# Kernel tuning notes

Hardware: AMD Instinct MI355X
Metric: run time of the kernel (lower is better)

## Reference

```python
import jax, jax.numpy as jnp
import numpy as np

N = 50000          # number of graph nodes
R = 4              # number of relation types (rt_num)
E = 800000         # edges per relation (avg degree 16)
D_IN = 128
D_OUT = 64
EPS = 1e-12        # torch F.normalize eps


def setup_inputs() -> dict:
    key = jax.random.key(0)
    k1, k2, k3, k4, k5 = jax.random.split(key, 5)
    x = jax.random.normal(k1, (N, D_IN), dtype=jnp.float32)
    W = jax.random.normal(k2, (R, D_IN, D_OUT), dtype=jnp.float32)
    b = jnp.zeros((R, D_OUT), dtype=jnp.float32)
    adj_vals = jax.random.uniform(k3, (R, E), dtype=jnp.float32)
    adj_rows = jax.random.randint(k4, (R, E), 0, N, dtype=jnp.int32)
    adj_cols = jax.random.randint(k5, (R, E), 0, N, dtype=jnp.int32)
    return {"x": x, "W": W, "b": b, "adj_vals": adj_vals,
            "adj_rows": adj_rows, "adj_cols": adj_cols, "dropout": 0}


def reference(x, W, b, adj_vals, adj_rows, adj_cols, dropout):
    # dropout == 0 -> F.dropout is the identity; reference is deterministic.
    # Per-relation dense projection: xw[r] = x @ W[r]   -> [R, N, D_OUT]
    xw = jnp.einsum('nd,rdo->rno', x, W)

    def per_relation(xw_r, rows_r, cols_r, vals_r, b_r):
        # sparse adjacency SpMM: out[i] = sum_e vals[e] * xw[cols[e]] for rows[e]==i
        msg = xw_r[cols_r] * vals_r[:, None]                  # [E, D_OUT] gather
        agg = jax.ops.segment_sum(msg, rows_r, num_segments=N)  # [N, D_OUT] scatter-add
        return jax.nn.relu(agg + b_r)                          # bias + act

    outs = jax.vmap(per_relation)(xw, adj_rows, adj_cols, adj_vals, b)  # [R, N, D_OUT]
    total = jnp.sum(outs, axis=0)                               # cross-relation sum
    # L2 normalize over feature dim (torch F.normalize, dim=1)
    norm = jnp.maximum(jnp.linalg.norm(total, axis=1, keepdims=True), EPS)
    return total / norm
```

## Files before the change

### kernel.cpp

```cpp
#include <hip/hip_runtime.h>
#include <hip/hip_bf16.h>
#include <stdint.h>

#define NN 50000
#define DI 128
#define DO 64
#define NE 800000
#define NR 4
#define NB 782
#define NBUCK (NR*NB)
#define PCHUNK 7168
#define PWG ((NE + PCHUNK - 1) / PCHUNK)
#define RSCAP 4096
#define CONVB 1024
#define GEMMB ((NN + 127) / 128)

typedef short short8 __attribute__((ext_vector_type(8)));
typedef float f32x4  __attribute__((ext_vector_type(4)));
union FragU { uint4 u; short8 s; };

__device__ __forceinline__ uint32_t bfb(float f)
{
    __hip_bfloat16 h = __float2bfloat16(f);
    return (uint32_t)*reinterpret_cast<unsigned short*>(&h);
}

template<int N, int PER, int BLK>
__device__ inline void block_exscan(int* a)
{
    __shared__ int wsum[BLK / 64];
    int tid = threadIdx.x;
    int base = tid * PER;
    int v[PER]; int s = 0;
    #pragma unroll
    for (int j = 0; j < PER; ++j) {
        int idx = base + j;
        int x = (idx < N) ? a[idx] : 0;
        v[j] = s; s += x;
    }
    int lane = tid & 63, wv = tid >> 6;
    int inc = s;
    #pragma unroll
    for (int off = 1; off < 64; off <<= 1) {
        int u = __shfl_up(inc, off);
        if (lane >= off) inc += u;
    }
    if (lane == 63) wsum[wv] = inc;
    __syncthreads();
    int woff = 0;
    for (int w = 0; w < wv; ++w) woff += wsum[w];
    int tb = woff + inc - s;
    #pragma unroll
    for (int j = 0; j < PER; ++j) {
        int idx = base + j;
        if (idx < N) a[idx] = tb + v[j];
    }
}

__global__ __launch_bounds__(256) void prep_kernel(
    const float* __restrict__ x, const float* __restrict__ W,
    const int* __restrict__ rows,
    uint2* __restrict__ xb, uint16_t* __restrict__ wt,
    int* __restrict__ gtot)
{
    __shared__ int h[NB];
    int bid = blockIdx.x, tid = threadIdx.x;

    if (bid < CONVB) {
        const int total = NN * DI / 4;
        const float4* x4 = (const float4*)x;
        for (int i = bid * 256 + tid; i < total; i += CONVB * 256) {
            float4 v = x4[i];
            uint2 o;
            o.x = bfb(v.x) | (bfb(v.y) << 16);
            o.y = bfb(v.z) | (bfb(v.w) << 16);
            xb[i] = o;
        }
    } else if (bid < CONVB + 128) {
        int i = (bid - CONVB) * 256 + tid;
        int r = i >> 13;
        int k = (i >> 6) & 127;
        int n = i & 63;
        wt[((size_t)(r * DO + n) << 7) + k] = (uint16_t)bfb(W[i]);
    } else {
        int bb = bid - (CONVB + 128);
        int r = bb >> 5, sub = bb & 31;
        for (int i = tid; i < NB; i += 256) h[i] = 0;
        __syncthreads();
        const int4* rr4 = (const int4*)(rows + (size_t)r * NE);
        for (int k = sub * 256 + tid; k < NE / 4; k += 32 * 256) {
            int4 v = rr4[k];
            atomicAdd(&h[v.x >> 6], 1);
            atomicAdd(&h[v.y >> 6], 1);
            atomicAdd(&h[v.z >> 6], 1);
            atomicAdd(&h[v.w >> 6], 1);
        }
        __syncthreads();
        int* gt = gtot + r * NB;
        for (int i = tid; i < NB; i += 256)
            if (h[i]) atomicAdd(&gt[i], h[i]);
    }
}

__global__ __launch_bounds__(512) void gemm_bases_kernel(
    const uint4* __restrict__ xb4, const uint4* __restrict__ wt4,
    uint16_t* __restrict__ xwb,
    const int* __restrict__ gtot, int* __restrict__ gstart,
    int* __restrict__ gcur)
{
    __shared__ __align__(16) uint16_t tile[128 * 64];
    __shared__ int a[NBUCK + 1];
    int tid = threadIdx.x;

    if (blockIdx.x == GEMMB) {
        for (int i = tid; i < NBUCK + 1; i += 512)
            a[i] = (i < NBUCK) ? gtot[i] : 0;
        __syncthreads();
        block_exscan<NBUCK + 1, 7, 512>(a);
        __syncthreads();
        for (int i = tid; i < NBUCK + 1; i += 512) {
            gstart[i] = a[i];
            if (i < NBUCK) gcur[i] = a[i];
        }
        return;
    }

    int wv = __builtin_amdgcn_readfirstlane(tid >> 6);
    int lane = tid & 63;
    int n0 = blockIdx.x * 128 + wv * 16;
    int m16 = lane & 15, g = lane >> 4;
    bool act = (n0 < NN);

    FragU af[4];
    if (act) {
        #pragma unroll
        for (int ks = 0; ks < 4; ++ks)
            af[ks].u = xb4[(size_t)(n0 + m16) * 16 + ks * 4 + g];
    }

    int rows = NN - blockIdx.x * 128; if (rows > 128) rows = 128;

    for (int r = 0; r < NR; ++r) {
        if (act) {
            #pragma unroll
            for (int ct = 0; ct < 4; ++ct) {
                f32x4 acc = {0.f, 0.f, 0.f, 0.f};
                #pragma unroll
                for (int ks = 0; ks < 4; ++ks) {
                    FragU b;
                    b.u = wt4[(size_t)((r * DO + ct * 16 + m16) * 16) + ks * 4 + g];
                    acc = __builtin_amdgcn_mfma_f32_16x16x32_bf16(
                        af[ks].s, b.s, acc, 0, 0, 0);
                }
                #pragma unroll
                for (int j = 0; j < 4; ++j)
                    tile[(wv * 16 + g * 4 + j) * 64 + ct * 16 + m16] =
                        (uint16_t)bfb(acc[j]);
            }
        }
        __syncthreads();
        uint4* dst = (uint4*)(xwb + ((size_t)r * NN + blockIdx.x * 128) * 64);
        int tot = rows * 8;
        for (int i = tid; i < tot; i += 512)
            dst[i] = ((const uint4*)tile)[i];
        __syncthreads();
    }
}

__global__ __launch_bounds__(512) void place_kernel(
    const int* __restrict__ rows, const int* __restrict__ cols,
    const float* __restrict__ vals, int* __restrict__ gcur,
    int2* __restrict__ csr)
{
    __shared__ int lofs[NB + 1];
    __shared__ int gbase[NB];
    __shared__ int2 stag[PCHUNK];
    int r = blockIdx.y;
    int tid = threadIdx.x;
    int e0 = blockIdx.x * PCHUNK;
    int cnt = NE - e0; if (cnt > PCHUNK) cnt = PCHUNK;
    const int*   rr = rows + (size_t)r * NE + e0;
    const int*   cc = cols + (size_t)r * NE + e0;
    const float* vv = vals + (size_t)r * NE + e0;

    for (int i = tid; i <= NB; i += 512) lofs[i] = 0;
    __syncthreads();
    for (int k = tid; k < cnt; k += 512) atomicAdd(&lofs[rr[k] >> 6], 1);
    __syncthreads();
    block_exscan<NB + 1, 2, 512>(lofs);
    __syncthreads();
    for (int b = tid; b < NB; b += 512) {
        int c = lofs[b + 1] - lofs[b];
        if (c > 0) gbase[b] = atomicAdd(&gcur[r * NB + b], c);
    }
    __syncthreads();
    for (int k = tid; k < cnt; k += 512) {
        int row = rr[k];
        int b = row >> 6;
        int slot = atomicAdd(&lofs[b], 1);
        stag[slot] = make_int2((cc[k] & 0xFFFF) | ((row & 63) << 16) | (b << 22),
                               __float_as_int(vv[k]));
    }
    __syncthreads();
    for (int i = tid; i < cnt; i += 512) {
        int2 t = stag[i];
        unsigned b2 = ((unsigned)t.x) >> 22;
        int start = b2 ? lofs[b2 - 1] : 0;
        csr[gbase[b2] + (i - start)] = t;
    }
}

__global__ __launch_bounds__(256) void rowsort_kernel(
    int2* __restrict__ csr, const int* __restrict__ gstart,
    int* __restrict__ rowptr)
{
    __shared__ int2 stag[RSCAP];
    __shared__ int cnt[64];
    __shared__ int ofs[64];
    int blk = blockIdx.x;
    int r   = blockIdx.y;
    int b   = r * NB + blk;
    int s = gstart[b], e = gstart[b + 1];
    int cntE = e - s; if (cntE > RSCAP) cntE = RSCAP;
    int tid = threadIdx.x;
    if (tid < 64) cnt[tid] = 0;
    __syncthreads();

    int2 ed[RSCAP / 256];
    #pragma unroll
    for (int j = 0; j < RSCAP / 256; ++j) {
        int i = tid + j * 256;
        if (i < cntE) {
            ed[j] = csr[s + i];
            atomicAdd(&cnt[(ed[j].x >> 16) & 63], 1);
        }
    }
    __syncthreads();
    if (tid < 64) {
        int c = cnt[tid];
        int inc = c;
        #pragma unroll
        for (int off = 1; off < 64; off <<= 1) {
            int u = __shfl_up(inc, off);
            if (tid >= off) inc += u;
        }
        ofs[tid] = inc - c;
        int n = blk * 64 + tid;
        if (n < NN) rowptr[(size_t)r * NN + n] = s + inc - c;
        if (b == NBUCK - 1 && tid == 0)
            rowptr[(size_t)NR * NN] = gstart[NBUCK];
    }
    __syncthreads();
    #pragma unroll
    for (int j = 0; j < RSCAP / 256; ++j) {
        int i = tid + j * 256;
        if (i < cntE) {
            int rl = (ed[j].x >> 16) & 63;
            int slot = atomicAdd(&ofs[rl], 1);
            stag[slot] = ed[j];
        }
    }
    __syncthreads();
    for (int i = tid; i < cntE; i += 256) {
        int2 t = stag[i];
        t.x = (r * NN + (t.x & 0xFFFF)) << 4;
        csr[s + i] = t;
    }
}

struct Stage {
    float v[NR];
    uint2 u[NR];
};

__device__ __forceinline__ void stage_issue(
    int k, const int* dege, const int* ofsv, const float* valv,
    const uint2* __restrict__ xw2, int e4, int fq, Stage& st)
{
    #pragma unroll
    for (int r = 0; r < NR; ++r) {
        if (k < dege[r]) {
            int ec = k + e4;
            int ofs  = __shfl(ofsv[r], ec);
            float vv = __shfl(valv[r], ec);
            st.v[r] = vv;
            st.u[r] = xw2[ofs + fq];
        } else {
            st.v[r] = 0.f;
            st.u[r] = make_uint2(0u, 0u);
        }
    }
}

__device__ __forceinline__ void stage_consume(const Stage& st, float a[NR][4])
{
    #pragma unroll
    for (int r = 0; r < NR; ++r) {
        float v = st.v[r];
        a[r][0] = fmaf(v, __uint_as_float(st.u[r].x << 16),          a[r][0]);
        a[r][1] = fmaf(v, __uint_as_float(st.u[r].x & 0xFFFF0000u),  a[r][1]);
        a[r][2] = fmaf(v, __uint_as_float(st.u[r].y << 16),          a[r][2]);
        a[r][3] = fmaf(v, __uint_as_float(st.u[r].y & 0xFFFF0000u),  a[r][3]);
    }
}

__global__ __launch_bounds__(256) void spmm_fused_kernel(
    const uint2* __restrict__ xw2, const int2* __restrict__ csr,
    const int* __restrict__ rowptr, const float* __restrict__ bias,
    float* __restrict__ out)
{
    int n = __builtin_amdgcn_readfirstlane(
        (int)((blockIdx.x * 256 + threadIdx.x) >> 6));
    int lane = threadIdx.x & 63;
    int e4 = lane >> 4, fq = lane & 15;
    if (n >= NN) return;

    int dege[NR]; int ofsv[NR]; float valv[NR];
    int sbeg[NR], send[NR];
    int maxdeg = 0;
    #pragma unroll
    for (int r = 0; r < NR; ++r) {
        sbeg[r] = rowptr[(size_t)r * NN + n];
        send[r] = rowptr[(size_t)r * NN + n + 1];
        int d = send[r] - sbeg[r];
        if (d > 64) d = 64;
        int2 cv = (lane < d) ? csr[sbeg[r] + lane] : make_int2(0, 0);
        ofsv[r] = cv.x;
        valv[r] = __int_as_float(cv.y);
        dege[r] = (d + 3) & ~3;
        maxdeg = max(maxdeg, dege[r]);
    }

    float a[NR][4];
    #pragma unroll
    for (int r = 0; r < NR; ++r)
        #pragma unroll
        for (int j = 0; j < 4; ++j) a[r][j] = 0.f;

    Stage A, B;
    stage_issue(0, dege, ofsv, valv, xw2, e4, fq, A);
    for (int k = 0; k < maxdeg; k += 8) {
        stage_issue(k + 4, dege, ofsv, valv, xw2, e4, fq, B);
        stage_consume(A, a);
        stage_issue(k + 8, dege, ofsv, valv, xw2, e4, fq, A);
        stage_consume(B, a);
    }

    #pragma unroll
    for (int r = 0; r < NR; ++r) {
        for (int i = sbeg[r] + 64; i < send[r]; ++i) {
            int2 cv = csr[i];
            float v = (lane < 16) ? __int_as_float(cv.y) : 0.f;
            uint2 u = xw2[cv.x + fq];
            a[r][0] = fmaf(v, __uint_as_float(u.x << 16),         a[r][0]);
            a[r][1] = fmaf(v, __uint_as_float(u.x & 0xFFFF0000u), a[r][1]);
            a[r][2] = fmaf(v, __uint_as_float(u.y << 16),         a[r][2]);
            a[r][3] = fmaf(v, __uint_as_float(u.y & 0xFFFF0000u), a[r][3]);
        }
    }

    float t[4] = {0.f, 0.f, 0.f, 0.f};
    #pragma unroll
    for (int r = 0; r < NR; ++r) {
        #pragma unroll
        for (int j = 0; j < 4; ++j) {
            a[r][j] += __shfl_xor(a[r][j], 16);
            a[r][j] += __shfl_xor(a[r][j], 32);
        }
        float4 br = *(const float4*)&bias[r * DO + 4 * fq];
        t[0] += fmaxf(a[r][0] + br.x, 0.f);
        t[1] += fmaxf(a[r][1] + br.y, 0.f);
        t[2] += fmaxf(a[r][2] + br.z, 0.f);
        t[3] += fmaxf(a[r][3] + br.w, 0.f);
    }
    float s2 = t[0]*t[0] + t[1]*t[1] + t[2]*t[2] + t[3]*t[3];
    #pragma unroll
    for (int off = 8; off >= 1; off >>= 1) s2 += __shfl_xor(s2, off);
    float inv = 1.0f / fmaxf(sqrtf(s2), 1e-12f);
    if (lane < 16) {
        float4 o = make_float4(t[0]*inv, t[1]*inv, t[2]*inv, t[3]*inv);
        *(float4*)&out[(size_t)n * DO + 4 * fq] = o;
    }
}

__global__ __launch_bounds__(256) void gemm_kernel(
    const float* __restrict__ x, const float* __restrict__ W,
    __hip_bfloat16* __restrict__ xwb)
{
    __shared__ float Wl[DI * DO];
    for (int i = threadIdx.x; i < DI * DO; i += 256) Wl[i] = W[i];
    __syncthreads();

    int wv   = __builtin_amdgcn_readfirstlane((int)(threadIdx.x >> 6));
    int lane = threadIdx.x & 63;
    int n0   = blockIdx.x * 32 + wv * 8;
    if (n0 >= NN) return;
    int nrows = NN - n0; if (nrows > 8) nrows = 8;

    if (nrows == 8) {
        const float* xr = x + (size_t)n0 * DI;
        float acc[8] = {0.f,0.f,0.f,0.f,0.f,0.f,0.f,0.f};
        #pragma unroll 8
        for (int k = 0; k < DI; ++k) {
            float w = Wl[k * DO + lane];
            #pragma unroll
            for (int rr = 0; rr < 8; ++rr)
                acc[rr] = fmaf(xr[(size_t)rr * DI + k], w, acc[rr]);
        }
        #pragma unroll
        for (int rr = 0; rr < 8; ++rr)
            xwb[(size_t)(n0 + rr) * DO + lane] = __float2bfloat16(acc[rr]);
    } else {
        for (int rr = 0; rr < nrows; ++rr) {
            const float* xr = x + (size_t)(n0 + rr) * DI;
            float acc = 0.f;
            for (int k = 0; k < DI; ++k)
                acc = fmaf(xr[k], Wl[k * DO + lane], acc);
            xwb[(size_t)(n0 + rr) * DO + lane] = __float2bfloat16(acc);
        }
    }
}

__global__ __launch_bounds__(256) void scatter_kernel(
    const __hip_bfloat16* __restrict__ xwb, const float* __restrict__ vals,
    const int* __restrict__ rows, const int* __restrict__ cols,
    float* __restrict__ agg)
{
    const int nPairs = NE / 2;
    int gwave  = (blockIdx.x * 256 + threadIdx.x) >> 6;
    int half   = (threadIdx.x >> 5) & 1;
    int l32    = threadIdx.x & 31;
    int stride = gridDim.x * 4;
    const uint16_t* xw16 = reinterpret_cast<const uint16_t*>(xwb);
    for (int p = gwave; p < nPairs; p += stride) {
        int e = 2 * p + half;
        int row = rows[e]; int col = cols[e]; float v = vals[e];
        uint32_t packed = *reinterpret_cast<const uint32_t*>(
            xw16 + ((size_t)col << 6) + 2 * l32);
        float f0 = __uint_as_float(packed << 16);
        float f1 = __uint_as_float(packed & 0xFFFF0000u);
        float* dst = agg + ((size_t)row << 6) + 2 * l32;
        atomicAdd(dst,     v * f0);
        atomicAdd(dst + 1, v * f1);
    }
}

__global__ __launch_bounds__(256) void accum_kernel(
    float* __restrict__ agg, const float* __restrict__ b,
    float* __restrict__ out, int first)
{
    int i = blockIdx.x * 256 + threadIdx.x;
    if (i >= NN * DO) return;
    float v = agg[i] + b[i & (DO - 1)];
    agg[i] = 0.f;
    v = fmaxf(v, 0.f);
    out[i] = first ? v : (out[i] + v);
}

__global__ __launch_bounds__(256) void norm_kernel(float* __restrict__ out)
{
    int n = (blockIdx.x * 256 + threadIdx.x) >> 6;
    int lane = threadIdx.x & 63;
    if (n >= NN) return;
    size_t idx = (size_t)n * DO + lane;
    float t = out[idx];
    float s = t * t;
    #pragma unroll
    for (int off = 32; off >= 1; off >>= 1) s += __shfl_xor(s, off);
    out[idx] = t / fmaxf(sqrtf(s), 1e-12f);
}

extern "C" void kernel_launch(void* const* d_in, const int* in_sizes, int n_in,
                              void* d_out, int out_size, void* d_ws, size_t ws_size,
                              hipStream_t stream)
{
    const float* x    = (const float*)d_in[0];
    const float* W    = (const float*)d_in[1];
    const float* b    = (const float*)d_in[2];
    const float* vals = (const float*)d_in[3];
    const int*   rows = (const int*)d_in[4];
    const int*   cols = (const int*)d_in[5];
    float* out = (float*)d_out;
    char* ws = (char*)d_ws;

    const size_t O_XW = 0;
    const size_t O_CS = O_XW + (size_t)NR * NN * DO * 2;
    const size_t O_RP = O_CS + (size_t)NR * NE * 8;
    const size_t O_GT = O_RP + ((size_t)NR * NN + 4) * 4;
    const size_t O_GS = O_GT + (size_t)NBUCK * 4;
    const size_t O_GC = O_GS + (size_t)(NBUCK + 1) * 4;
    const size_t NEED = O_GC + (size_t)NBUCK * 4;
    const size_t O_XB = O_CS;
    const size_t O_WT = O_CS + 13u * 1024 * 1024;

    if (ws_size >= NEED) {
        __hip_bfloat16* xwb = (__hip_bfloat16*)(ws + O_XW);
        int2* csr   = (int2*)(ws + O_CS);
        int* rowptr = (int*)(ws + O_RP);
        int* gtot   = (int*)(ws + O_GT);
        int* gstart = (int*)(ws + O_GS);
        int* gcur   = (int*)(ws + O_GC);
        uint2* xb   = (uint2*)(ws + O_XB);
        uint16_t* wt = (uint16_t*)(ws + O_WT);

        hipMemsetAsync(gtot, 0, (size_t)NBUCK * 4, stream);
        prep_kernel<<<dim3(CONVB + 128 + 128), dim3(256), 0, stream>>>(
            x, W, rows, xb, wt, gtot);
        gemm_bases_kernel<<<dim3(GEMMB + 1), dim3(512), 0, stream>>>(
            (const uint4*)xb, (const uint4*)wt, (uint16_t*)xwb,
            gtot, gstart, gcur);
        place_kernel<<<dim3(PWG, NR), dim3(512), 0, stream>>>(
            rows, cols, vals, gcur, csr);
        rowsort_kernel<<<dim3(NB, NR), dim3(256), 0, stream>>>(csr, gstart, rowptr);
        spmm_fused_kernel<<<dim3((NN * 64 + 255) / 256), dim3(256), 0, stream>>>(
            (const uint2*)xwb, csr, rowptr, b, out);
    } else {
        __hip_bfloat16* xwb = (__hip_bfloat16*)ws;
        float* agg = (float*)(ws + (size_t)NN * DO * 2);
        hipMemsetAsync(agg, 0, (size_t)NN * DO * 4, stream);
        for (int r = 0; r < NR; ++r) {
            gemm_kernel<<<dim3((NN + 31) / 32), dim3(256), 0, stream>>>(
                x, W + (size_t)r * DI * DO, xwb);
            scatter_kernel<<<dim3(2048), dim3(256), 0, stream>>>(
                xwb, vals + (size_t)r * NE, rows + (size_t)r * NE,
                cols + (size_t)r * NE, agg);
            accum_kernel<<<dim3((NN * DO + 255) / 256), dim3(256), 0, stream>>>(
                agg, b + (size_t)r * DO, out, r == 0);
        }
        norm_kernel<<<dim3((NN * DO + 255) / 256), dim3(256), 0, stream>>>(out);
    }
}
```

Measured before the change: 178.6 us.

## Fuse x bf16 conversion into GEMM and co-schedule GEMM with edge placement

Removes the separate x-to-bf16 conversion pass: the GEMM now loads fp32 x directly and converts to bf16 fragments in registers. The GEMM blocks are merged into one launch with the edge-placement blocks, so the two independent phases run concurrently, and the bucket prefix-scan becomes its own single-block kernel. This avoids writing and re-reading an intermediate bf16 copy of x and some launch serialization. In exchange it adds a tiny extra launch and a large shared-memory footprint for every block of the merged kernel, which may limit occupancy for the GEMM blocks.

```diff
diff --git a/kernel.cpp b/kernel.cpp
--- a/kernel.cpp
+++ b/kernel.cpp
@@ -12,7 +12,6 @@
 #define PCHUNK 7168
 #define PWG ((NE + PCHUNK - 1) / PCHUNK)
 #define RSCAP 4096
-#define CONVB 1024
 #define GEMMB ((NN + 127) / 128)
 
 typedef short short8 __attribute__((ext_vector_type(8)));
@@ -58,32 +57,20 @@
 }
 
 __global__ __launch_bounds__(256) void prep_kernel(
-    const float* __restrict__ x, const float* __restrict__ W,
-    const int* __restrict__ rows,
-    uint2* __restrict__ xb, uint16_t* __restrict__ wt,
-    int* __restrict__ gtot)
+    const float* __restrict__ W, const int* __restrict__ rows,
+    uint16_t* __restrict__ wt, int* __restrict__ gtot)
 {
     __shared__ int h[NB];
     int bid = blockIdx.x, tid = threadIdx.x;
 
-    if (bid < CONVB) {
-        const int total = NN * DI / 4;
-        const float4* x4 = (const float4*)x;
-        for (int i = bid * 256 + tid; i < total; i += CONVB * 256) {
-            float4 v = x4[i];
-            uint2 o;
-            o.x = bfb(v.x) | (bfb(v.y) << 16);
-            o.y = bfb(v.z) | (bfb(v.w) << 16);
-            xb[i] = o;
-        }
-    } else if (bid < CONVB + 128) {
-        int i = (bid - CONVB) * 256 + tid;
+    if (bid < 128) {
+        int i = bid * 256 + tid;
         int r = i >> 13;
         int k = (i >> 6) & 127;
         int n = i & 63;
         wt[((size_t)(r * DO + n) << 7) + k] = (uint16_t)bfb(W[i]);
     } else {
-        int bb = bid - (CONVB + 128);
+        int bb = bid - 128;
         int r = bb >> 5, sub = bb & 31;
         for (int i = tid; i < NB; i += 256) h[i] = 0;
         __syncthreads();
@@ -102,82 +89,92 @@
     }
 }
 
-__global__ __launch_bounds__(512) void gemm_bases_kernel(
-    const uint4* __restrict__ xb4, const uint4* __restrict__ wt4,
-    uint16_t* __restrict__ xwb,
+__global__ __launch_bounds__(512) void bases_kernel(
     const int* __restrict__ gtot, int* __restrict__ gstart,
     int* __restrict__ gcur)
 {
-    __shared__ __align__(16) uint16_t tile[128 * 64];
     __shared__ int a[NBUCK + 1];
     int tid = threadIdx.x;
-
-    if (blockIdx.x == GEMMB) {
-        for (int i = tid; i < NBUCK + 1; i += 512)
-            a[i] = (i < NBUCK) ? gtot[i] : 0;
-        __syncthreads();
-        block_exscan<NBUCK + 1, 7, 512>(a);
-        __syncthreads();
-        for (int i = tid; i < NBUCK + 1; i += 512) {
-            gstart[i] = a[i];
-            if (i < NBUCK) gcur[i] = a[i];
-        }
-        return;
-    }
-
-    int wv = __builtin_amdgcn_readfirstlane(tid >> 6);
-    int lane = tid & 63;
-    int n0 = blockIdx.x * 128 + wv * 16;
-    int m16 = lane & 15, g = lane >> 4;
-    bool act = (n0 < NN);
-
-    FragU af[4];
-    if (act) {
-        #pragma unroll
-        for (int ks = 0; ks < 4; ++ks)
-            af[ks].u = xb4[(size_t)(n0 + m16) * 16 + ks * 4 + g];
-    }
-
-    int rows = NN - blockIdx.x * 128; if (rows > 128) rows = 128;
-
-    for (int r = 0; r < NR; ++r) {
-        if (act) {
-            #pragma unroll
-            for (int ct = 0; ct < 4; ++ct) {
-                f32x4 acc = {0.f, 0.f, 0.f, 0.f};
-                #pragma unroll
-                for (int ks = 0; ks < 4; ++ks) {
-                    FragU b;
-                    b.u = wt4[(size_t)((r * DO + ct * 16 + m16) * 16) + ks * 4 + g];
-                    acc = __builtin_amdgcn_mfma_f32_16x16x32_bf16(
-                        af[ks].s, b.s, acc, 0, 0, 0);
-                }
-                #pragma unroll
-                for (int j = 0; j < 4; ++j)
-                    tile[(wv * 16 + g * 4 + j) * 64 + ct * 16 + m16] =
-                        (uint16_t)bfb(acc[j]);
-            }
-        }
-        __syncthreads();
-        uint4* dst = (uint4*)(xwb + ((size_t)r * NN + blockIdx.x * 128) * 64);
-        int tot = rows * 8;
-        for (int i = tid; i < tot; i += 512)
-            dst[i] = ((const uint4*)tile)[i];
-        __syncthreads();
-    }
-}
-
-__global__ __launch_bounds__(512) void place_kernel(
+    for (int i = tid; i < NBUCK + 1; i += 512) a[i] = (i < NBUCK) ? gtot[i] : 0;
+    __syncthreads();
+    block_exscan<NBUCK + 1, 7, 512>(a);
+    __syncthreads();
+    for (int i = tid; i < NBUCK + 1; i += 512) {
+        gstart[i] = a[i];
+        if (i < NBUCK) gcur[i] = a[i];
+    }
+}
+
+__global__ __launch_bounds__(512) void gemm_place_kernel(
+    const float* __restrict__ x, const uint4* __restrict__ wt4,
+    uint16_t* __restrict__ xwb,
     const int* __restrict__ rows, const int* __restrict__ cols,
     const float* __restrict__ vals, int* __restrict__ gcur,
     int2* __restrict__ csr)
 {
-    __shared__ int lofs[NB + 1];
-    __shared__ int gbase[NB];
-    __shared__ int2 stag[PCHUNK];
-    int r = blockIdx.y;
+    __shared__ __align__(16) char smem[63616];
     int tid = threadIdx.x;
-    int e0 = blockIdx.x * PCHUNK;
+
+    if (blockIdx.x < GEMMB) {
+        uint16_t* tile = (uint16_t*)smem;
+        int wv = __builtin_amdgcn_readfirstlane(tid >> 6);
+        int lane = tid & 63;
+        int n0 = blockIdx.x * 128 + wv * 16;
+        int m16 = lane & 15, g = lane >> 4;
+        bool act = (n0 < NN);
+
+        FragU af[4];
+        if (act) {
+            const float4* x4 = (const float4*)x;
+            size_t rb = ((size_t)(n0 + m16) * DI) >> 2;
+            #pragma unroll
+            for (int ks = 0; ks < 4; ++ks) {
+                float4 f0 = x4[rb + ks * 8 + g * 2];
+                float4 f1 = x4[rb + ks * 8 + g * 2 + 1];
+                af[ks].u.x = bfb(f0.x) | (bfb(f0.y) << 16);
+                af[ks].u.y = bfb(f0.z) | (bfb(f0.w) << 16);
+                af[ks].u.z = bfb(f1.x) | (bfb(f1.y) << 16);
+                af[ks].u.w = bfb(f1.z) | (bfb(f1.w) << 16);
+            }
+        }
+
+        int nrows = NN - blockIdx.x * 128; if (nrows > 128) nrows = 128;
+
+        for (int r = 0; r < NR; ++r) {
+            if (act) {
+                #pragma unroll
+                for (int ct = 0; ct < 4; ++ct) {
+                    f32x4 acc = {0.f, 0.f, 0.f, 0.f};
+                    #pragma unroll
+                    for (int ks = 0; ks < 4; ++ks) {
+                        FragU b;
+                        b.u = wt4[(size_t)((r * DO + ct * 16 + m16) * 16) + ks * 4 + g];
+                        acc = __builtin_amdgcn_mfma_f32_16x16x32_bf16(
+                            af[ks].s, b.s, acc, 0, 0, 0);
+                    }
+                    #pragma unroll
+                    for (int j = 0; j < 4; ++j)
+                        tile[(wv * 16 + g * 4 + j) * 64 + ct * 16 + m16] =
+                            (uint16_t)bfb(acc[j]);
+                }
+            }
+            __syncthreads();
+            uint4* dst = (uint4*)(xwb + ((size_t)r * NN + blockIdx.x * 128) * 64);
+            int tot = nrows * 8;
+            for (int i = tid; i < tot; i += 512)
+                dst[i] = ((const uint4*)tile)[i];
+            __syncthreads();
+        }
+        return;
+    }
+
+    int* lofs  = (int*)smem;
+    int* gbase = (int*)(smem + 3136);
+    int2* stag = (int2*)(smem + 6272);
+    int pb = blockIdx.x - GEMMB;
+    int r = pb / PWG;
+    int chunk = pb - r * PWG;
+    int e0 = chunk * PCHUNK;
     int cnt = NE - e0; if (cnt > PCHUNK) cnt = PCHUNK;
     const int*   rr = rows + (size_t)r * NE + e0;
     const int*   cc = cols + (size_t)r * NE + e0;
@@ -489,9 +486,8 @@
     const size_t O_GT = O_RP + ((size_t)NR * NN + 4) * 4;
     const size_t O_GS = O_GT + (size_t)NBUCK * 4;
     const size_t O_GC = O_GS + (size_t)(NBUCK + 1) * 4;
-    const size_t NEED = O_GC + (size_t)NBUCK * 4;
-    const size_t O_XB = O_CS;
-    const size_t O_WT = O_CS + 13u * 1024 * 1024;
+    const size_t O_WT = O_GC + (size_t)NBUCK * 4;
+    const size_t NEED = O_WT + 65536;
 
     if (ws_size >= NEED) {
         __hip_bfloat16* xwb = (__hip_bfloat16*)(ws + O_XW);
@@ -500,16 +496,13 @@
         int* gtot   = (int*)(ws + O_GT);
         int* gstart = (int*)(ws + O_GS);
         int* gcur   = (int*)(ws + O_GC);
-        uint2* xb   = (uint2*)(ws + O_XB);
         uint16_t* wt = (uint16_t*)(ws + O_WT);
 
         hipMemsetAsync(gtot, 0, (size_t)NBUCK * 4, stream);
-        prep_kernel<<<dim3(CONVB + 128 + 128), dim3(256), 0, stream>>>(
-            x, W, rows, xb, wt, gtot);
-        gemm_bases_kernel<<<dim3(GEMMB + 1), dim3(512), 0, stream>>>(
-            (const uint4*)xb, (const uint4*)wt, (uint16_t*)xwb,
-            gtot, gstart, gcur);
-        place_kernel<<<dim3(PWG, NR), dim3(512), 0, stream>>>(
+        prep_kernel<<<dim3(256), dim3(256), 0, stream>>>(W, rows, wt, gtot);
+        bases_kernel<<<dim3(1), dim3(512), 0, stream>>>(gtot, gstart, gcur);
+        gemm_place_kernel<<<dim3(GEMMB + PWG * NR), dim3(512), 0, stream>>>(
+            x, (const uint4*)wt, (uint16_t*)xwb,
             rows, cols, vals, gcur, csr);
         rowsort_kernel<<<dim3(NB, NR), dim3(256), 0, stream>>>(csr, gstart, rowptr);
         spmm_fused_kernel<<<dim3((NN * 64 + 255) / 256), dim3(256), 0, stream>>>(
```

Result: faster. 171.9 us (-3.8%).
